# Performance work log

Hardware: AMD Instinct MI355X
Metric: run time of the kernel (lower is better)

The kernel has to match this reference:

```python
import jax, jax.numpy as jnp
import numpy as np

HIDDEN = 512
HEADS = 8
DK = HIDDEN // HEADS  # 64
NEG = -1000000000.0


def setup_inputs() -> dict:
    key = jax.random.key(0)
    ks = jax.random.split(key, 16)
    B, S = 4, 1024
    inp = {
        "q": jax.random.normal(ks[0], (B, S, HIDDEN), jnp.float32),
        "k": jax.random.normal(ks[1], (B, S, HIDDEN), jnp.float32),
        "v": jax.random.normal(ks[2], (B, S, HIDDEN), jnp.float32),
        "attn_bias": jax.random.normal(ks[3], (B, HEADS, S, S), jnp.float32),
        "graph_mask": jax.random.randint(ks[4], (B, 1, S, S), 0, 2, jnp.int32),
        "subsq_mask": jax.random.normal(ks[5], (B, 1, S, S), jnp.float32),
        # linear params (PyTorch Linear: y = x @ W.T + b)
        "Wq": jax.random.normal(ks[6], (HIDDEN, HIDDEN), jnp.float32) * 0.02,
        "bq": jnp.zeros((HIDDEN,), jnp.float32),
        "Wk": jax.random.normal(ks[7], (HIDDEN, HIDDEN), jnp.float32) * 0.02,
        "bk": jnp.zeros((HIDDEN,), jnp.float32),
        "Wv": jax.random.normal(ks[8], (HIDDEN, HIDDEN), jnp.float32) * 0.02,
        "bv": jnp.zeros((HIDDEN,), jnp.float32),
        "Wo": jax.random.normal(ks[9], (HIDDEN, HIDDEN), jnp.float32) * 0.02,
        "bo": jnp.zeros((HIDDEN,), jnp.float32),
    }
    return inp


def reference(q, k, v, attn_bias, graph_mask, subsq_mask, Wq, bq, Wk, bk, Wv, bv, Wo, bo):
    B, S, _ = q.shape
    scale = DK ** (-0.5)
    # projections -> [B, heads, S, d]
    qh = (q @ Wq.T + bq).reshape(B, S, HEADS, DK).transpose(0, 2, 1, 3)
    kh = (k @ Wk.T + bk).reshape(B, S, HEADS, DK).transpose(0, 2, 1, 3)
    vh = (v @ Wv.T + bv).reshape(B, S, HEADS, DK).transpose(0, 2, 1, 3)
    # scaled scores [B, heads, S, S]
    scores = jnp.einsum('bhqd,bhkd->bhqk', qh * scale, kh)
    zero = graph_mask == 0  # [B,1,S,S], broadcasts over heads
    bias = jnp.where(zero, NEG, attn_bias)
    x = scores + bias + subsq_mask
    x = jnp.where(zero, NEG, x)
    attn = jax.nn.softmax(x, axis=-1)
    out = jnp.einsum('bhqk,bhkd->bhqd', attn, vh)
    out = out.transpose(0, 2, 1, 3).reshape(B, S, HEADS * DK)
    return out @ Wo.T + bo
```

## Files before the change

### kernel.cpp

```cpp
#include <hip/hip_runtime.h>

#define HIDDEN 512
#define HEADS 8
#define DK 64
#define S_ 1024
#define NEGV -1000000000.0f

typedef _Float16 half8 __attribute__((ext_vector_type(8)));
typedef _Float16 half4 __attribute__((ext_vector_type(4)));
typedef _Float16 half2_t __attribute__((ext_vector_type(2)));
typedef float f32x4 __attribute__((ext_vector_type(4)));
typedef float f32x2 __attribute__((ext_vector_type(2)));
typedef int i32x4 __attribute__((ext_vector_type(4)));

__device__ __forceinline__ void gload16(const void* g, void* l) {
  __builtin_amdgcn_global_load_lds(
      (const __attribute__((address_space(1))) unsigned int*)g,
      (__attribute__((address_space(3))) unsigned int*)l, 16, 0, 0);
}

__global__ __launch_bounds__(256) void prep(
    const float* __restrict__ q, const float* __restrict__ k,
    const float* __restrict__ v,
    const float* __restrict__ Wq, const float* __restrict__ Wk,
    const float* __restrict__ Wv, const float* __restrict__ Wo,
    const int* __restrict__ gm, const float* __restrict__ sq,
    _Float16* q16, _Float16* k16, _Float16* v16,
    _Float16* wq16, _Float16* wk16, _Float16* wv16, _Float16* wo16,
    _Float16* msk) {
  int blk = blockIdx.x;
  if (blk < 6144) {
    int job = blk / 2048, rel = blk % 2048;
    const float* src = job == 0 ? q : (job == 1 ? k : v);
    _Float16* dst = job == 0 ? q16 : (job == 1 ? k16 : v16);
    int i = (rel * 256 + threadIdx.x) * 4;
    float4 vv = *(const float4*)(src + i);
    half4 h = {(_Float16)vv.x, (_Float16)vv.y, (_Float16)vv.z, (_Float16)vv.w};
    *(half4*)(dst + i) = h;
  } else if (blk < 7168) {
    int job = (blk - 6144) / 256, rel = (blk - 6144) % 256;
    const float* src = job == 0 ? Wq : (job == 1 ? Wk : (job == 2 ? Wv : Wo));
    _Float16* dst = job == 0 ? wq16 : (job == 1 ? wk16 : (job == 2 ? wv16 : wo16));
    int i = (rel * 256 + threadIdx.x) * 4;
    float4 vv = *(const float4*)(src + i);
    half4 h = {(_Float16)vv.x, (_Float16)vv.y, (_Float16)vv.z, (_Float16)vv.w};
    *(half4*)(dst + i) = h;
  } else {
    int rel = blk - 7168;
    int i = (rel * 256 + threadIdx.x) * 4;
    i32x4 g = *(const i32x4*)(gm + i);
    f32x4 s = *(const f32x4*)(sq + i);
    half4 o;
#pragma unroll
    for (int j = 0; j < 4; j++)
      o[j] = (_Float16)(g[j] == 0 ? -30000.0f : s[j]);
    *(half4*)(msk + i) = o;
  }
}

__global__ __launch_bounds__(256) void proj_qkv2(
    const _Float16* __restrict__ q16, const _Float16* __restrict__ k16,
    const _Float16* __restrict__ v16,
    const _Float16* __restrict__ wq, const _Float16* __restrict__ wk,
    const _Float16* __restrict__ wv,
    const float* __restrict__ bq, const float* __restrict__ bk,
    const float* __restrict__ bv,
    _Float16* __restrict__ qh, _Float16* __restrict__ kh, _Float16* __restrict__ vt) {
  int m0 = blockIdx.x * 64;
  int nb = blockIdx.y;
  int which = nb >> 3;
  int n0 = (nb & 7) * 64;
  const _Float16* X = which == 0 ? q16 : (which == 1 ? k16 : v16);
  const _Float16* W = which == 0 ? wq : (which == 1 ? wk : wv);
  const float* bias = which == 0 ? bq : (which == 1 ? bk : bv);

  int tid = threadIdx.x;
  int wave = tid >> 6, lane = tid & 63;
  int r16 = lane & 15, quad = lane >> 4;

  __shared__ __align__(16) char SM[25600];
  _Float16(*T)[72] = (_Float16(*)[72])(SM + 16384);

  int rl = lane >> 2;
  int ku = lane & 3;
  int kup = ku ^ ((rl >> 1) & 3);

  const _Float16* Xg = X + (size_t)(m0 + wave * 16 + rl) * HIDDEN + kup * 8;
  const _Float16* Wg = W + (size_t)(n0 + wave * 16 + rl) * HIDDEN + kup * 8;

  auto stage = [&](int k0, int buf) __attribute__((always_inline)) {
    gload16(Xg + k0, SM + buf * 4096 + wave * 1024);
    gload16(Wg + k0, SM + 8192 + buf * 4096 + wave * 1024);
  };

  f32x4 acc[4] = {};
  stage(0, 0);
  int sw = (r16 >> 1) & 3;

  auto compute = [&](int t) __attribute__((always_inline)) {
    int buf = t & 1;
    const _Float16* XT = (const _Float16*)(SM + buf * 4096);
    const _Float16* WT = (const _Float16*)(SM + 8192 + buf * 4096);
    half8 a = *(const half8*)&XT[(wave * 16 + r16) * 32 + ((quad ^ sw) << 3)];
#pragma unroll
    for (int nt = 0; nt < 4; nt++) {
      half8 bfr = *(const half8*)&WT[(nt * 16 + r16) * 32 + ((quad ^ sw) << 3)];
      acc[nt] = __builtin_amdgcn_mfma_f32_16x16x32_f16(a, bfr, acc[nt], 0, 0, 0);
    }
  };

  for (int t = 0; t < 15; t++) {
    stage((t + 1) * 32, (t + 1) & 1);
    asm volatile("s_waitcnt vmcnt(2)" ::: "memory");
    __builtin_amdgcn_sched_barrier(0);
    __builtin_amdgcn_s_barrier();
    compute(t);
    __builtin_amdgcn_s_barrier();
  }
  asm volatile("s_waitcnt vmcnt(0)" ::: "memory");
  __builtin_amdgcn_sched_barrier(0);
  __builtin_amdgcn_s_barrier();
  compute(15);

  if (which < 2) {
    _Float16* OUT = which == 0 ? qh : kh;
    float scale = which == 0 ? 0.125f : 1.0f;
#pragma unroll
    for (int nt = 0; nt < 4; nt++) {
      int gcol = n0 + nt * 16 + r16;
      float bv_ = bias[gcol];
      int h = gcol >> 6, d = gcol & 63;
#pragma unroll
      for (int r = 0; r < 4; r++) {
        int grow = m0 + wave * 16 + quad * 4 + r;
        int bb = grow >> 10, s = grow & 1023;
        float val = (acc[nt][r] + bv_) * scale;
        OUT[((bb * HEADS + h) * S_ + s) * DK + d] = (_Float16)val;
      }
    }
  } else {
#pragma unroll
    for (int nt = 0; nt < 4; nt++) {
      int lc = nt * 16 + r16;
      float bv_ = bias[n0 + lc];
#pragma unroll
      for (int r = 0; r < 4; r++) {
        int lr = wave * 16 + quad * 4 + r;
        T[lr][lc] = (_Float16)(acc[nt][r] + bv_);
      }
    }
    __syncthreads();
    int dl = tid >> 2;
    int s4 = (tid & 3) * 16;
    _Float16 tmp[16];
#pragma unroll
    for (int i = 0; i < 16; i++) tmp[i] = T[s4 + i][dl];
    int h = n0 >> 6;
    int bb = m0 >> 10;
    int s0 = m0 & 1023;
    _Float16* p = vt + ((bb * HEADS + h) * DK + dl) * S_ + s0 + s4;
    *(half8*)(p) = *(half8*)(tmp);
    *(half8*)(p + 8) = *(half8*)(tmp + 8);
  }
}

__global__ __launch_bounds__(512) void attn13(
    const _Float16* __restrict__ qh, const _Float16* __restrict__ kh,
    const _Float16* __restrict__ vt,
    const float* __restrict__ attn_bias, const _Float16* __restrict__ msk,
    _Float16* __restrict__ ao) {
  int id = blockIdx.x;
  int bh = (((id >> 3) & 3) << 3) | (id & 7);
  int qtile = id >> 5;
  int b = bh >> 3, h = bh & 7;
  int tid = threadIdx.x;
  int wave = tid >> 6, lane = tid & 63;
  int col = lane & 15, quad = lane >> 4;
  int q0w = qtile * 128 + wave * 16;
  int q = q0w + col;
  int xr = col & 7;
  int lr8 = lane >> 3;
  int u8 = (lane & 7) ^ lr8;

  __shared__ __align__(16) char SMEM[141312];
  unsigned(*P2)[16][20] = (unsigned(*)[16][20])(SMEM + 131072);

  const _Float16* Q = qh + ((size_t)bh * S_ + q) * DK;
  const _Float16* K = kh + (size_t)bh * S_ * DK;
  const _Float16* V = vt + (size_t)bh * DK * S_;
  const float* BIrow = attn_bias + ((size_t)bh * S_ + q0w) * S_;
  const _Float16* MSrow = msk + ((size_t)b * S_ + q0w) * S_;

  half8 qf0 = *(const half8*)(Q + quad * 8);
  half8 qf1 = *(const half8*)(Q + 32 + quad * 8);

  f32x4 acc[4] = {};
  float m_r = -1e38f, l_r = 0.0f;

  auto stage_clump = [&](int tt, int buf) __attribute__((always_inline)) {
    int kb = tt * 64;
    {
      int row = wave * 8 + lr8;
      gload16(K + (size_t)(kb + row) * DK + u8 * 8,
              SMEM + buf * 8192 + wave * 1024);
      gload16(V + (size_t)row * S_ + kb + u8 * 8,
              SMEM + 16384 + buf * 8192 + wave * 1024);
    }
#pragma unroll
    for (int c = 0; c < 4; c++) {
      int row = c * 4 + (lane >> 4);
      int ju = (lane & 15) ^ (row & 7);
      gload16(BIrow + (size_t)row * S_ + kb + ju * 4,
              SMEM + 32768 + buf * 32768 + wave * 4096 + c * 1024);
    }
#pragma unroll
    for (int c = 0; c < 2; c++) {
      int row = c * 8 + lr8;
      gload16(MSrow + (size_t)row * S_ + kb + u8 * 8,
              SMEM + 98304 + buf * 16384 + wave * 2048 + c * 1024);
    }
  };

  auto compute = [&](int t) __attribute__((always_inline)) {
    int buf = t & 1;
    _Float16* Klds = (_Float16*)(SMEM + buf * 8192);
    _Float16* Vlds = (_Float16*)(SMEM + 16384 + buf * 8192);
    float* Bw = (float*)(SMEM + 32768 + buf * 32768 + wave * 4096);
    _Float16* Mw = (_Float16*)(SMEM + 98304 + buf * 16384 + wave * 2048);

#pragma unroll
    for (int hf = 0; hf < 2; hf++) {
      int kcl = hf * 32;
      int R0 = kcl + col, R1 = kcl + 16 + col;
      half8 kf00 = *(const half8*)&Klds[R0 * 64 + ((quad ^ xr) << 3)];
      half8 kf01 = *(const half8*)&Klds[R0 * 64 + (((quad + 4) ^ xr) << 3)];
      half8 kf10 = *(const half8*)&Klds[R1 * 64 + ((quad ^ xr) << 3)];
      half8 kf11 = *(const half8*)&Klds[R1 * 64 + (((quad + 4) ^ xr) << 3)];

      int ku = (kcl >> 3) + quad;
      half8 vf0 = *(const half8*)&Vlds[(0 * 16 + col) * 64 + ((ku ^ xr) << 3)];
      half8 vf1 = *(const half8*)&Vlds[(1 * 16 + col) * 64 + ((ku ^ xr) << 3)];
      half8 vf2 = *(const half8*)&Vlds[(2 * 16 + col) * 64 + ((ku ^ xr) << 3)];
      half8 vf3 = *(const half8*)&Vlds[(3 * 16 + col) * 64 + ((ku ^ xr) << 3)];

      int jb = kcl >> 2;
      f32x4 bi0 = *(const f32x4*)&Bw[col * 64 + (((jb + quad) ^ xr) << 2)];
      f32x4 bi1 = *(const f32x4*)&Bw[col * 64 + (((jb + 4 + quad) ^ xr) << 2)];
      int jm = (kcl >> 3) + (quad >> 1);
      half4 mk0 = *(const half4*)&Mw[col * 64 + ((jm ^ xr) << 3) + (quad & 1) * 4];
      half4 mk1 = *(const half4*)&Mw[col * 64 + (((jm + 2) ^ xr) << 3) + (quad & 1) * 4];

      __builtin_amdgcn_s_setprio(1);
      f32x4 s0 = {}, s1 = {};
      s0 = __builtin_amdgcn_mfma_f32_16x16x32_f16(kf00, qf0, s0, 0, 0, 0);
      s0 = __builtin_amdgcn_mfma_f32_16x16x32_f16(kf01, qf1, s0, 0, 0, 0);
      s1 = __builtin_amdgcn_mfma_f32_16x16x32_f16(kf10, qf0, s1, 0, 0, 0);
      s1 = __builtin_amdgcn_mfma_f32_16x16x32_f16(kf11, qf1, s1, 0, 0, 0);
      __builtin_amdgcn_s_setprio(0);

      float x0[4], x1[4];
#pragma unroll
      for (int r = 0; r < 4; r++) {
        x0[r] = s0[r] + bi0[r] + (float)mk0[r];
        x1[r] = s1[r] + bi1[r] + (float)mk1[r];
      }

      float mx = fmaxf(fmaxf(fmaxf(x0[0], x0[1]), fmaxf(x0[2], x0[3])),
                       fmaxf(fmaxf(x1[0], x1[1]), fmaxf(x1[2], x1[3])));
      mx = fmaxf(mx, __shfl_xor(mx, 16));
      mx = fmaxf(mx, __shfl_xor(mx, 32));
      float mnew = fmaxf(m_r, mx);
      float f = __expf(m_r - mnew);
      float p0[4], p1[4];
      float ps = 0.0f;
#pragma unroll
      for (int r = 0; r < 4; r++) {
        p0[r] = __expf(x0[r] - mnew);
        p1[r] = __expf(x1[r] - mnew);
        ps += p0[r] + p1[r];
      }
      ps += __shfl_xor(ps, 16);
      ps += __shfl_xor(ps, 32);
      l_r = l_r * f + ps;
      m_r = mnew;
#pragma unroll
      for (int nt = 0; nt < 4; nt++) acc[nt] *= f;

      half2_t c0 = {(_Float16)p0[0], (_Float16)p0[1]};
      half2_t c1 = {(_Float16)p0[2], (_Float16)p0[3]};
      half2_t c2 = {(_Float16)p1[0], (_Float16)p1[1]};
      half2_t c3 = {(_Float16)p1[2], (_Float16)p1[3]};
      P2[wave][col][quad * 2 + 0] = __builtin_bit_cast(unsigned, c0);
      P2[wave][col][quad * 2 + 1] = __builtin_bit_cast(unsigned, c1);
      P2[wave][col][8 + quad * 2 + 0] = __builtin_bit_cast(unsigned, c2);
      P2[wave][col][8 + quad * 2 + 1] = __builtin_bit_cast(unsigned, c3);

      half8 pf = *(const half8*)&P2[wave][col][quad * 4];

      __builtin_amdgcn_s_setprio(1);
      acc[0] = __builtin_amdgcn_mfma_f32_16x16x32_f16(vf0, pf, acc[0], 0, 0, 0);
      acc[1] = __builtin_amdgcn_mfma_f32_16x16x32_f16(vf1, pf, acc[1], 0, 0, 0);
      acc[2] = __builtin_amdgcn_mfma_f32_16x16x32_f16(vf2, pf, acc[2], 0, 0, 0);
      acc[3] = __builtin_amdgcn_mfma_f32_16x16x32_f16(vf3, pf, acc[3], 0, 0, 0);
      __builtin_amdgcn_s_setprio(0);
    }
  };

  stage_clump(0, 0);

  for (int t = 0; t < 15; t++) {
    stage_clump(t + 1, (t + 1) & 1);
    asm volatile("s_waitcnt vmcnt(8)" ::: "memory");
    __builtin_amdgcn_sched_barrier(0);
    __builtin_amdgcn_s_barrier();
    compute(t);
    __builtin_amdgcn_s_barrier();
  }
  asm volatile("s_waitcnt vmcnt(0)" ::: "memory");
  __builtin_amdgcn_sched_barrier(0);
  __builtin_amdgcn_s_barrier();
  compute(15);

  float linv = 1.0f / l_r;
  _Float16* aop = ao + (size_t)(b * S_ + q) * HIDDEN + h * DK;
#pragma unroll
  for (int nt = 0; nt < 4; nt++)
#pragma unroll
    for (int rp = 0; rp < 2; rp++) {
      int d = nt * 16 + quad * 4 + rp * 2;
      half2_t o = {(_Float16)(acc[nt][rp * 2] * linv),
                   (_Float16)(acc[nt][rp * 2 + 1] * linv)};
      *(half2_t*)(aop + d) = o;
    }
}

__global__ __launch_bounds__(256) void out_proj2(
    const _Float16* __restrict__ ao, const _Float16* __restrict__ wo,
    const float* __restrict__ bo, float* __restrict__ out) {
  int m0 = blockIdx.x * 64;
  int n0 = blockIdx.y * 64;
  int tid = threadIdx.x, wave = tid >> 6, lane = tid & 63;
  int r16 = lane & 15, quad = lane >> 4;

  __shared__ __align__(16) char SM[16384];
  int rl = lane >> 2;
  int ku = lane & 3;
  int kup = ku ^ ((rl >> 1) & 3);

  const _Float16* Xg = ao + (size_t)(m0 + wave * 16 + rl) * HIDDEN + kup * 8;
  const _Float16* Wg = wo + (size_t)(n0 + wave * 16 + rl) * HIDDEN + kup * 8;

  auto stage = [&](int k0, int buf) __attribute__((always_inline)) {
    gload16(Xg + k0, SM + buf * 4096 + wave * 1024);
    gload16(Wg + k0, SM + 8192 + buf * 4096 + wave * 1024);
  };

  f32x4 acc[4] = {};
  stage(0, 0);
  int sw = (r16 >> 1) & 3;

  auto compute = [&](int t) __attribute__((always_inline)) {
    int buf = t & 1;
    const _Float16* XT = (const _Float16*)(SM + buf * 4096);
    const _Float16* WT = (const _Float16*)(SM + 8192 + buf * 4096);
    half8 a = *(const half8*)&XT[(wave * 16 + r16) * 32 + ((quad ^ sw) << 3)];
#pragma unroll
    for (int nt = 0; nt < 4; nt++) {
      half8 bfr = *(const half8*)&WT[(nt * 16 + r16) * 32 + ((quad ^ sw) << 3)];
      acc[nt] = __builtin_amdgcn_mfma_f32_16x16x32_f16(a, bfr, acc[nt], 0, 0, 0);
    }
  };

  for (int t = 0; t < 15; t++) {
    stage((t + 1) * 32, (t + 1) & 1);
    asm volatile("s_waitcnt vmcnt(2)" ::: "memory");
    __builtin_amdgcn_sched_barrier(0);
    __builtin_amdgcn_s_barrier();
    compute(t);
    __builtin_amdgcn_s_barrier();
  }
  asm volatile("s_waitcnt vmcnt(0)" ::: "memory");
  __builtin_amdgcn_sched_barrier(0);
  __builtin_amdgcn_s_barrier();
  compute(15);

#pragma unroll
  for (int nt = 0; nt < 4; nt++) {
    int gcol = n0 + nt * 16 + r16;
    float bv_ = bo[gcol];
#pragma unroll
    for (int r = 0; r < 4; r++) {
      int grow = m0 + wave * 16 + quad * 4 + r;
      out[grow * HIDDEN + gcol] = acc[nt][r] + bv_;
    }
  }
}

extern "C" void kernel_launch(void* const* d_in, const int* in_sizes, int n_in,
                              void* d_out, int out_size, void* d_ws, size_t ws_size,
                              hipStream_t stream) {
  const float* q = (const float*)d_in[0];
  const float* k = (const float*)d_in[1];
  const float* v = (const float*)d_in[2];
  const float* attn_bias = (const float*)d_in[3];
  const int* gmask = (const int*)d_in[4];
  const float* subsq = (const float*)d_in[5];
  const float* Wq = (const float*)d_in[6];
  const float* bq = (const float*)d_in[7];
  const float* Wk = (const float*)d_in[8];
  const float* bk = (const float*)d_in[9];
  const float* Wv = (const float*)d_in[10];
  const float* bv = (const float*)d_in[11];
  const float* Wo = (const float*)d_in[12];
  const float* bo = (const float*)d_in[13];

  char* ws = (char*)d_ws;
  _Float16* q16 = (_Float16*)(ws + 0);
  _Float16* k16 = (_Float16*)(ws + 4194304);
  _Float16* v16 = (_Float16*)(ws + 8388608);
  _Float16* wq16 = (_Float16*)(ws + 12582912);
  _Float16* wk16 = (_Float16*)(ws + 13107200);
  _Float16* wv16 = (_Float16*)(ws + 13631488);
  _Float16* wo16 = (_Float16*)(ws + 14155776);
  _Float16* qhb = (_Float16*)(ws + 14680064);
  _Float16* khb = (_Float16*)(ws + 18874368);
  _Float16* vtb = (_Float16*)(ws + 23068672);
  _Float16* aob = (_Float16*)(ws + 27262976);
  _Float16* msk16 = (_Float16*)(ws + 31457280);

  prep<<<dim3(11264), 256, 0, stream>>>(q, k, v, Wq, Wk, Wv, Wo, gmask, subsq,
                                        q16, k16, v16, wq16, wk16, wv16, wo16,
                                        msk16);
  proj_qkv2<<<dim3(64, 24), 256, 0, stream>>>(q16, k16, v16, wq16, wk16, wv16,
                                              bq, bk, bv, qhb, khb, vtb);
  attn13<<<dim3(256), 512, 0, stream>>>(qhb, khb, vtb, attn_bias, msk16, aob);
  out_proj2<<<dim3(64, 8), 256, 0, stream>>>(aob, wo16, bo, (float*)d_out);
}
```

Measured before the change: 79.19 us.

## Load attention bias straight into registers with a two-tile-ahead prefetch

The attn_bias tile is no longer staged through LDS with global_load_lds. Each lane now loads its own bias values with vector global loads, two tiles ahead, using alternating register sets in a loop unrolled by two. This removes the bias LDS buffers (shared memory drops from about 141 KB to 76 KB) and the LDS reads for bias inside the compute step. In exchange it uses more registers and less coalesced global loads per row, and the vmcnt wait thresholds have to be adjusted by hand.

```diff
diff --git a/kernel.cpp b/kernel.cpp
--- a/kernel.cpp
+++ b/kernel.cpp
@@ -164,7 +164,11 @@
   }
 }
 
-__global__ __launch_bounds__(512) void attn13(
+struct BiasR {
+  f32x4 b00, b01, b10, b11;
+};
+
+__global__ __launch_bounds__(512) void attn15(
     const _Float16* __restrict__ qh, const _Float16* __restrict__ kh,
     const _Float16* __restrict__ vt,
     const float* __restrict__ attn_bias, const _Float16* __restrict__ msk,
@@ -182,13 +186,13 @@
   int lr8 = lane >> 3;
   int u8 = (lane & 7) ^ lr8;
 
-  __shared__ __align__(16) char SMEM[141312];
-  unsigned(*P2)[16][20] = (unsigned(*)[16][20])(SMEM + 131072);
+  __shared__ __align__(16) char SMEM[75776];
+  unsigned(*P2)[16][20] = (unsigned(*)[16][20])(SMEM + 65536);
 
   const _Float16* Q = qh + ((size_t)bh * S_ + q) * DK;
   const _Float16* K = kh + (size_t)bh * S_ * DK;
   const _Float16* V = vt + (size_t)bh * DK * S_;
-  const float* BIrow = attn_bias + ((size_t)bh * S_ + q0w) * S_;
+  const float* BI = attn_bias + ((size_t)bh * S_ + q) * S_;
   const _Float16* MSrow = msk + ((size_t)b * S_ + q0w) * S_;
 
   half8 qf0 = *(const half8*)(Q + quad * 8);
@@ -207,26 +211,28 @@
               SMEM + 16384 + buf * 8192 + wave * 1024);
     }
 #pragma unroll
-    for (int c = 0; c < 4; c++) {
-      int row = c * 4 + (lane >> 4);
-      int ju = (lane & 15) ^ (row & 7);
-      gload16(BIrow + (size_t)row * S_ + kb + ju * 4,
-              SMEM + 32768 + buf * 32768 + wave * 4096 + c * 1024);
-    }
-#pragma unroll
     for (int c = 0; c < 2; c++) {
       int row = c * 8 + lr8;
       gload16(MSrow + (size_t)row * S_ + kb + u8 * 8,
-              SMEM + 98304 + buf * 16384 + wave * 2048 + c * 1024);
-    }
-  };
-
-  auto compute = [&](int t) __attribute__((always_inline)) {
+              SMEM + 32768 + buf * 16384 + wave * 2048 + c * 1024);
+    }
+  };
+
+  auto loadB = [&](int tt) __attribute__((always_inline)) -> BiasR {
+    int kc = tt * 64;
+    BiasR r;
+    r.b00 = *(const f32x4*)(BI + kc + quad * 4);
+    r.b01 = *(const f32x4*)(BI + kc + 16 + quad * 4);
+    r.b10 = *(const f32x4*)(BI + kc + 32 + quad * 4);
+    r.b11 = *(const f32x4*)(BI + kc + 48 + quad * 4);
+    return r;
+  };
+
+  auto compute = [&](int t, const BiasR& BR) __attribute__((always_inline)) {
     int buf = t & 1;
     _Float16* Klds = (_Float16*)(SMEM + buf * 8192);
     _Float16* Vlds = (_Float16*)(SMEM + 16384 + buf * 8192);
-    float* Bw = (float*)(SMEM + 32768 + buf * 32768 + wave * 4096);
-    _Float16* Mw = (_Float16*)(SMEM + 98304 + buf * 16384 + wave * 2048);
+    _Float16* Mw = (_Float16*)(SMEM + 32768 + buf * 16384 + wave * 2048);
 
 #pragma unroll
     for (int hf = 0; hf < 2; hf++) {
@@ -243,9 +249,8 @@
       half8 vf2 = *(const half8*)&Vlds[(2 * 16 + col) * 64 + ((ku ^ xr) << 3)];
       half8 vf3 = *(const half8*)&Vlds[(3 * 16 + col) * 64 + ((ku ^ xr) << 3)];
 
-      int jb = kcl >> 2;
-      f32x4 bi0 = *(const f32x4*)&Bw[col * 64 + (((jb + quad) ^ xr) << 2)];
-      f32x4 bi1 = *(const f32x4*)&Bw[col * 64 + (((jb + 4 + quad) ^ xr) << 2)];
+      f32x4 bi0 = hf == 0 ? BR.b00 : BR.b10;
+      f32x4 bi1 = hf == 0 ? BR.b01 : BR.b11;
       int jm = (kcl >> 3) + (quad >> 1);
       half4 mk0 = *(const half4*)&Mw[col * 64 + ((jm ^ xr) << 3) + (quad & 1) * 4];
       half4 mk1 = *(const half4*)&Mw[col * 64 + (((jm + 2) ^ xr) << 3) + (quad & 1) * 4];
@@ -307,19 +312,59 @@
   };
 
   stage_clump(0, 0);
-
-  for (int t = 0; t < 15; t++) {
-    stage_clump(t + 1, (t + 1) & 1);
-    asm volatile("s_waitcnt vmcnt(8)" ::: "memory");
-    __builtin_amdgcn_sched_barrier(0);
-    __builtin_amdgcn_s_barrier();
-    compute(t);
-    __builtin_amdgcn_s_barrier();
-  }
+  BiasR bA = loadB(0);
+  BiasR bB = loadB(1);
+
+#pragma unroll 1
+  for (int it = 0; it < 7; it++) {
+    int t = it * 2;
+    {
+      stage_clump(t + 1, (t + 1) & 1);
+      f32x4 n0, n1, n2, n3;
+      {
+        int kc = (t + 2) * 64;
+        n0 = *(const f32x4*)(BI + kc + quad * 4);
+        n1 = *(const f32x4*)(BI + kc + 16 + quad * 4);
+        n2 = *(const f32x4*)(BI + kc + 32 + quad * 4);
+        n3 = *(const f32x4*)(BI + kc + 48 + quad * 4);
+      }
+      asm volatile("s_waitcnt vmcnt(12)" ::: "memory");
+      __builtin_amdgcn_sched_barrier(0);
+      __builtin_amdgcn_s_barrier();
+      compute(t, bA);
+      bA.b00 = n0; bA.b01 = n1; bA.b10 = n2; bA.b11 = n3;
+      __builtin_amdgcn_s_barrier();
+    }
+    {
+      stage_clump(t + 2, (t + 2) & 1);
+      f32x4 n0, n1, n2, n3;
+      {
+        int kc = (t + 3) * 64;
+        n0 = *(const f32x4*)(BI + kc + quad * 4);
+        n1 = *(const f32x4*)(BI + kc + 16 + quad * 4);
+        n2 = *(const f32x4*)(BI + kc + 32 + quad * 4);
+        n3 = *(const f32x4*)(BI + kc + 48 + quad * 4);
+      }
+      asm volatile("s_waitcnt vmcnt(12)" ::: "memory");
+      __builtin_amdgcn_sched_barrier(0);
+      __builtin_amdgcn_s_barrier();
+      compute(t + 1, bB);
+      bB.b00 = n0; bB.b01 = n1; bB.b10 = n2; bB.b11 = n3;
+      __builtin_amdgcn_s_barrier();
+    }
+  }
+
+  stage_clump(15, 1);
+  asm volatile("s_waitcnt vmcnt(8)" ::: "memory");
+  __builtin_amdgcn_sched_barrier(0);
+  __builtin_amdgcn_s_barrier();
+  compute(14, bA);
+  __builtin_amdgcn_s_barrier();
+
   asm volatile("s_waitcnt vmcnt(0)" ::: "memory");
   __builtin_amdgcn_sched_barrier(0);
   __builtin_amdgcn_s_barrier();
-  compute(15);
+  compute(15, bB);
 
   float linv = 1.0f / l_r;
   _Float16* aop = ao + (size_t)(b * S_ + q) * HIDDEN + h * DK;
@@ -433,6 +478,6 @@
                                         msk16);
   proj_qkv2<<<dim3(64, 24), 256, 0, stream>>>(q16, k16, v16, wq16, wk16, wv16,
                                               bq, bk, bv, qhb, khb, vtb);
-  attn13<<<dim3(256), 512, 0, stream>>>(qhb, khb, vtb, attn_bias, msk16, aob);
+  attn15<<<dim3(256), 512, 0, stream>>>(qhb, khb, vtb, attn_bias, msk16, aob);
   out_proj2<<<dim3(64, 8), 256, 0, stream>>>(aob, wo16, bo, (float*)d_out);
 }
```

Result: no change. 79.60 us (+0.5%).
